# Kernel tuning notes

Hardware: AMD Instinct MI355X
Metric: run time of the kernel (lower is better)

## Reference

```python
import jax, jax.numpy as jnp
import numpy as np

B, NQ, NK, DQ, DK, D = 32, 1024, 2048, 256, 256, 256


def setup_inputs() -> dict:
    key = jax.random.key(0)
    ks = jax.random.split(key, 12)
    s = lambda fan_in: 1.0 / np.sqrt(fan_in)
    return {
        "query_input": jax.random.normal(ks[0], (B, NQ, DQ), jnp.float32),
        "key_input": jax.random.normal(ks[1], (B, NK, DK), jnp.float32),
        "value_input": jax.random.normal(ks[2], (B, NK, DK), jnp.float32),
        "query_input_mask": jax.random.randint(ks[3], (B, NQ), 0, 2).astype(jnp.int32),
        "key_input_mask": jax.random.randint(ks[4], (B, NK), 0, 2).astype(jnp.int32),
        "attn_bias": jax.random.normal(ks[5], (B, NQ, NK), jnp.float32),
        "Wq": jax.random.uniform(ks[6], (D, DQ), jnp.float32, -s(DQ), s(DQ)),
        "bq": jax.random.uniform(ks[7], (D,), jnp.float32, -s(DQ), s(DQ)),
        "Wk": jax.random.uniform(ks[8], (D, DK), jnp.float32, -s(DK), s(DK)),
        "bk": jax.random.uniform(ks[9], (D,), jnp.float32, -s(DK), s(DK)),
        "Wv": jax.random.uniform(ks[10], (D, DK), jnp.float32, -s(DK), s(DK)),
        "bv": jax.random.uniform(ks[11], (D,), jnp.float32, -s(DK), s(DK)),
    }


def reference(query_input, key_input, value_input, query_input_mask, key_input_mask,
              attn_bias, Wq, bq, Wk, bk, Wv, bv):
    scale = float(D) ** 0.5
    q = jnp.einsum("bqi,di->bqd", query_input, Wq) + bq  # (B, Nq, D)
    k = jnp.einsum("bki,di->bkd", key_input, Wk) + bk    # (B, Nk, D)
    v = jnp.einsum("bki,di->bkd", value_input, Wv) + bv  # (B, Nk, D)
    logits = jnp.einsum("bqd,bkd->bqk", q, k) / scale + attn_bias  # (B, Nq, Nk)
    # attn_mask[b,q,k] = query_mask[b,q] * key_mask[b,k]; masked_fill where == 0
    mask = (query_input_mask[:, :, None] * key_input_mask[:, None, :]) != 0
    logits = jnp.where(mask, logits, jnp.asarray(-1e9, logits.dtype))
    weights = jax.nn.softmax(logits, axis=-1)
    out = jnp.einsum("bqk,bkd->bqd", weights, v)
    return (out, weights)
```

## Files before the change

kernel.cpp:

```cpp
#include <hip/hip_runtime.h>
#include <stdint.h>

#define NB 32
#define NQd 1024
#define NKd 2048
#define DDd 256

typedef __attribute__((ext_vector_type(4))) float f32x4;
typedef __attribute__((ext_vector_type(8))) short s16x8;

__device__ __forceinline__ unsigned short f2bf(float f) {
  unsigned int u = __builtin_bit_cast(unsigned int, f);
  u += 0x7fffu + ((u >> 16) & 1u);
  return (unsigned short)(u >> 16);
}

template <int MODE>
__global__ __launch_bounds__(512) void proj_kernel(
    const float* __restrict__ P, const float* __restrict__ Q,
    const float* __restrict__ bias, unsigned short* __restrict__ out) {
  __shared__ __align__(16) char lds[32768];
  char* Pl = lds;
  char* Ql = lds + 16384;

  const int tid = threadIdx.x;
  const int m0 = blockIdx.x * 128, n0 = blockIdx.y * 128;
  const int lane = tid & 63, w = tid >> 6;
  const int lr = lane & 15, lg = lane >> 4;
  const int wm = w >> 2, wn = w & 3;

  f32x4 acc[4][2];
#pragma unroll
  for (int a = 0; a < 4; a++)
#pragma unroll
    for (int b2 = 0; b2 < 2; b2++) acc[a][b2] = (f32x4){0.f, 0.f, 0.f, 0.f};

  for (int k0 = 0; k0 < 256; k0 += 64) {
    __syncthreads();
#pragma unroll
    for (int j = 0; j < 2; j++) {
      int c = tid + j * 512;
      int row = c >> 3, cc = c & 7;
      int dst = row * 128 + ((cc * 16) ^ ((row & 7) << 4));
      {
        const float* src = P + (size_t)(m0 + row) * 256 + k0 + cc * 8;
        f32x4 x = *(const f32x4*)src;
        f32x4 y = *(const f32x4*)(src + 4);
        s16x8 pk;
        pk[0] = (short)f2bf(x[0]); pk[1] = (short)f2bf(x[1]);
        pk[2] = (short)f2bf(x[2]); pk[3] = (short)f2bf(x[3]);
        pk[4] = (short)f2bf(y[0]); pk[5] = (short)f2bf(y[1]);
        pk[6] = (short)f2bf(y[2]); pk[7] = (short)f2bf(y[3]);
        *(s16x8*)(Pl + dst) = pk;
      }
      {
        const float* src = Q + (size_t)(n0 + row) * 256 + k0 + cc * 8;
        f32x4 x = *(const f32x4*)src;
        f32x4 y = *(const f32x4*)(src + 4);
        s16x8 pk;
        pk[0] = (short)f2bf(x[0]); pk[1] = (short)f2bf(x[1]);
        pk[2] = (short)f2bf(x[2]); pk[3] = (short)f2bf(x[3]);
        pk[4] = (short)f2bf(y[0]); pk[5] = (short)f2bf(y[1]);
        pk[6] = (short)f2bf(y[2]); pk[7] = (short)f2bf(y[3]);
        *(s16x8*)(Ql + dst) = pk;
      }
    }
    __syncthreads();
#pragma unroll
    for (int ks = 0; ks < 2; ks++) {
      s16x8 af[4], bf[2];
      int kbyte = ks * 64 + lg * 16;
#pragma unroll
      for (int fm = 0; fm < 4; fm++) {
        int row = wm * 64 + fm * 16 + lr;
        af[fm] = *(const s16x8*)(Pl + row * 128 + (kbyte ^ ((row & 7) << 4)));
      }
#pragma unroll
      for (int fn = 0; fn < 2; fn++) {
        int row = wn * 32 + fn * 16 + lr;
        bf[fn] = *(const s16x8*)(Ql + row * 128 + (kbyte ^ ((row & 7) << 4)));
      }
#pragma unroll
      for (int fm = 0; fm < 4; fm++)
#pragma unroll
        for (int fn = 0; fn < 2; fn++)
          acc[fm][fn] = __builtin_amdgcn_mfma_f32_16x16x32_bf16(
              af[fm], bf[fn], acc[fm][fn], 0, 0, 0);
    }
  }

  if (MODE == 0) {
    float bv[2];
#pragma unroll
    for (int fn = 0; fn < 2; fn++) bv[fn] = bias[n0 + wn * 32 + fn * 16 + lr];
#pragma unroll
    for (int fm = 0; fm < 4; fm++)
#pragma unroll
      for (int i = 0; i < 4; i++) {
        int m = m0 + wm * 64 + fm * 16 + lg * 4 + i;
#pragma unroll
        for (int fn = 0; fn < 2; fn++) {
          int n = n0 + wn * 32 + fn * 16 + lr;
          out[(size_t)m * 256 + n] = f2bf(acc[fm][fn][i] + bv[fn]);
        }
      }
  } else {
#pragma unroll
    for (int fm = 0; fm < 4; fm++)
#pragma unroll
      for (int i = 0; i < 4; i++) {
        int m = m0 + wm * 64 + fm * 16 + lg * 4 + i;
        float bm = bias[m];
#pragma unroll
        for (int fn = 0; fn < 2; fn++) {
          int n = n0 + wn * 32 + fn * 16 + lr;
          int bb = n >> 11, nn = n & 2047;
          out[(size_t)bb * 524288 + (size_t)m * 2048 + nn] =
              f2bf(acc[fm][fn][i] + bm);
        }
      }
  }
}

__global__ __launch_bounds__(512) void attn_kernel(
    const unsigned short* __restrict__ qb, const unsigned short* __restrict__ kb,
    const unsigned short* __restrict__ vT, const int* __restrict__ qmask,
    const int* __restrict__ kmask, const float* __restrict__ bias,
    float* __restrict__ out, float* __restrict__ weights,
    float* __restrict__ rowsum_ws) {
  __shared__ __align__(16) char lds[65536];
  char* Kl = lds;
  char* Vl = lds + 32768;
  char* Sl = lds;
  float* rowsum_lds = (float*)lds;

  int bid = blockIdx.x;
  int swz = (bid & 7) * 64 + (bid >> 3);
  int b = swz >> 4, qt = swz & 15;
  int q0 = qt * 64;
  const int tid = threadIdx.x, lane = tid & 63, w = tid >> 6;
  const int lr = lane & 15, lg = lane >> 4;
  const int wm = w >> 2, wn = w & 3;

  s16x8 qf[2][8];
  {
    const unsigned short* qbase =
        qb + (size_t)(b * 1024 + q0 + wm * 32 + lr) * 256 + lg * 8;
#pragma unroll
    for (int fm = 0; fm < 2; fm++)
#pragma unroll
      for (int ks = 0; ks < 8; ks++)
        qf[fm][ks] = *(const s16x8*)(qbase + fm * 16 * 256 + ks * 32);
  }
  unsigned qmbits = 0;
#pragma unroll
  for (int fm = 0; fm < 2; fm++)
#pragma unroll
    for (int i = 0; i < 4; i++) {
      int qm = qmask[b * 1024 + q0 + wm * 32 + fm * 16 + lg * 4 + i];
      qmbits |= (qm ? 1u : 0u) << (fm * 4 + i);
    }

  f32x4 acc_o[2][4];
#pragma unroll
  for (int a = 0; a < 2; a++)
#pragma unroll
    for (int c = 0; c < 4; c++) acc_o[a][c] = (f32x4){0.f, 0.f, 0.f, 0.f};
  float rs[2][4];
#pragma unroll
  for (int a = 0; a < 2; a++)
#pragma unroll
    for (int i = 0; i < 4; i++) rs[a][i] = 0.f;

  const size_t kb_base = (size_t)b * 2048 * 256;
  const size_t vT_base = (size_t)b * 256 * 2048;

  for (int kt = 0; kt < 32; kt++) {
    __syncthreads();
#pragma unroll
    for (int j = 0; j < 4; j++) {
      int c = tid + j * 512;
      {
        int row = c >> 5, cb = (c & 31) * 16;
        s16x8 kv = *(const s16x8*)(kb + kb_base +
                                   (size_t)(kt * 64 + row) * 256 + (cb >> 1));
        *(s16x8*)(Kl + row * 512 + (cb ^ ((row & 7) << 4))) = kv;
      }
      {
        int row = c >> 3, cb = (c & 7) * 16;
        s16x8 vv = *(const s16x8*)(vT + vT_base + (size_t)row * 2048 +
                                   kt * 64 + (cb >> 1));
        *(s16x8*)(Vl + row * 128 + (cb ^ ((row & 7) << 4))) = vv;
      }
    }
    __syncthreads();
    f32x4 sacc[2];
    sacc[0] = (f32x4){0.f, 0.f, 0.f, 0.f};
    sacc[1] = (f32x4){0.f, 0.f, 0.f, 0.f};
    {
      int krow = wn * 16 + lr;
      int swzk = (krow & 7) << 4;
#pragma unroll
      for (int ks = 0; ks < 8; ks++) {
        s16x8 bfr = *(const s16x8*)(Kl + krow * 512 + ((ks * 64 + lg * 16) ^ swzk));
        sacc[0] = __builtin_amdgcn_mfma_f32_16x16x32_bf16(qf[0][ks], bfr, sacc[0], 0, 0, 0);
        sacc[1] = __builtin_amdgcn_mfma_f32_16x16x32_bf16(qf[1][ks], bfr, sacc[1], 0, 0, 0);
      }
    }
    __syncthreads();
    {
      int kcol = kt * 64 + wn * 16 + lr;
      int km = kmask[b * 2048 + kcol];
#pragma unroll
      for (int fm = 0; fm < 2; fm++)
#pragma unroll
        for (int i = 0; i < 4; i++) {
          int qrow = q0 + wm * 32 + fm * 16 + lg * 4 + i;
          float lgt = sacc[fm][i] * 0.0625f +
                      bias[((size_t)b * 1024 + qrow) * 2048 + kcol];
          float s;
          if (!((qmbits >> (fm * 4 + i)) & 1u))
            s = 1.0f;
          else
            s = km ? __expf(lgt) : 0.0f;
          rs[fm][i] += s;
          weights[((size_t)b * 1024 + qrow) * 2048 + kcol] = s;
          int srow = wm * 32 + fm * 16 + lg * 4 + i;
          int scol2 = (wn * 16 + lr) * 2;
          int sbyte = srow * 128 + ((scol2 & ~15) ^ ((srow & 7) << 4)) + (scol2 & 15);
          *(unsigned short*)(Sl + sbyte) = f2bf(s);
        }
    }
    __syncthreads();
#pragma unroll
    for (int ks = 0; ks < 2; ks++) {
      int kbyte = ks * 64 + lg * 16;
      s16x8 af[2], bfr[4];
#pragma unroll
      for (int fm = 0; fm < 2; fm++) {
        int row = wm * 32 + fm * 16 + lr;
        af[fm] = *(const s16x8*)(Sl + row * 128 + (kbyte ^ ((row & 7) << 4)));
      }
#pragma unroll
      for (int fn = 0; fn < 4; fn++) {
        int row = wn * 64 + fn * 16 + lr;
        bfr[fn] = *(const s16x8*)(Vl + row * 128 + (kbyte ^ ((row & 7) << 4)));
      }
#pragma unroll
      for (int fm = 0; fm < 2; fm++)
#pragma unroll
        for (int fn = 0; fn < 4; fn++)
          acc_o[fm][fn] = __builtin_amdgcn_mfma_f32_16x16x32_bf16(
              af[fm], bfr[fn], acc_o[fm][fn], 0, 0, 0);
    }
  }
  __syncthreads();
  if (tid < 64) rowsum_lds[tid] = 0.f;
  __syncthreads();
#pragma unroll
  for (int fm = 0; fm < 2; fm++)
#pragma unroll
    for (int i = 0; i < 4; i++) {
      float v = rs[fm][i];
      v += __shfl_xor(v, 1);
      v += __shfl_xor(v, 2);
      v += __shfl_xor(v, 4);
      v += __shfl_xor(v, 8);
      if (lr == 0) atomicAdd(&rowsum_lds[wm * 32 + fm * 16 + lg * 4 + i], v);
    }
  __syncthreads();
#pragma unroll
  for (int fm = 0; fm < 2; fm++)
#pragma unroll
    for (int i = 0; i < 4; i++) {
      int srow = wm * 32 + fm * 16 + lg * 4 + i;
      float rinv = 1.0f / rowsum_lds[srow];
      int qrow = q0 + srow;
#pragma unroll
      for (int fn = 0; fn < 4; fn++) {
        int d = wn * 64 + fn * 16 + lr;
        out[((size_t)b * 1024 + qrow) * 256 + d] = acc_o[fm][fn][i] * rinv;
      }
    }
  if (tid < 64) rowsum_ws[b * 1024 + q0 + tid] = rowsum_lds[tid];
}

__global__ __launch_bounds__(256) void rescale_kernel(
    float* __restrict__ weights, const float* __restrict__ rowsum) {
  const size_t total = (size_t)32 * 1024 * 2048 / 4;
  size_t stride = (size_t)gridDim.x * blockDim.x;
  for (size_t i = (size_t)blockIdx.x * blockDim.x + threadIdx.x; i < total;
       i += stride) {
    size_t row = i >> 9;
    float rinv = 1.0f / rowsum[row];
    f32x4 v = ((const f32x4*)weights)[i];
    v[0] *= rinv; v[1] *= rinv; v[2] *= rinv; v[3] *= rinv;
    ((f32x4*)weights)[i] = v;
  }
}

extern "C" void kernel_launch(void* const* d_in, const int* in_sizes, int n_in,
                              void* d_out, int out_size, void* d_ws,
                              size_t ws_size, hipStream_t stream) {
  const float* query = (const float*)d_in[0];
  const float* key = (const float*)d_in[1];
  const float* value = (const float*)d_in[2];
  const int* qmask = (const int*)d_in[3];
  const int* kmask = (const int*)d_in[4];
  const float* bias = (const float*)d_in[5];
  const float* Wq = (const float*)d_in[6];
  const float* bq = (const float*)d_in[7];
  const float* Wk = (const float*)d_in[8];
  const float* bk = (const float*)d_in[9];
  const float* Wv = (const float*)d_in[10];
  const float* bv = (const float*)d_in[11];

  float* out = (float*)d_out;
  float* weights = out + (size_t)32 * 1024 * 256;

  char* ws = (char*)d_ws;
  unsigned short* qb = (unsigned short*)ws;
  unsigned short* kbb = (unsigned short*)(ws + 16777216);
  unsigned short* vT = (unsigned short*)(ws + 50331648);
  float* rowsum = (float*)(ws + 83886080);

  proj_kernel<0><<<dim3(256, 2), 512, 0, stream>>>(query, Wq, bq, qb);
  proj_kernel<0><<<dim3(512, 2), 512, 0, stream>>>(key, Wk, bk, kbb);
  proj_kernel<1><<<dim3(2, 512), 512, 0, stream>>>(Wv, value, bv, vT);
  attn_kernel<<<dim3(512), 512, 0, stream>>>(qb, kbb, vT, qmask, kmask, bias,
                                             out, weights, rowsum);
  rescale_kernel<<<dim3(2048), 256, 0, stream>>>(weights, rowsum);
}
```

Baseline: 872.4 us.

## Stage logits through LDS for coalesced vectorized bias loads and weight stores

The attention kernel now writes raw QK scores to a rotated fp32 LDS tile and re-reads them in a row-major layout, so each thread handles four contiguous columns of one row. Bias loads, mask loads and weight stores become 16-byte coalesced nontemporal accesses, and the bias for the next tile is prefetched. The row sum is reduced with a short shuffle, and the kernel stores reciprocals so the rescale pass avoids divisions. This costs an extra LDS round-trip and barrier per tile, and adds a minBlocks launch bound that may constrain registers.

```diff
diff --git a/kernel.cpp b/kernel.cpp
--- a/kernel.cpp
+++ b/kernel.cpp
@@ -1,13 +1,10 @@
 #include <hip/hip_runtime.h>
 #include <stdint.h>
 
-#define NB 32
-#define NQd 1024
-#define NKd 2048
-#define DDd 256
-
 typedef __attribute__((ext_vector_type(4))) float f32x4;
 typedef __attribute__((ext_vector_type(8))) short s16x8;
+typedef __attribute__((ext_vector_type(4))) short s16x4;
+typedef __attribute__((ext_vector_type(4))) int i32x4;
 
 __device__ __forceinline__ unsigned short f2bf(float f) {
   unsigned int u = __builtin_bit_cast(unsigned int, f);
@@ -122,16 +119,17 @@
   }
 }
 
-__global__ __launch_bounds__(512) void attn_kernel(
+__global__ __launch_bounds__(512, 4) void attn_kernel(
     const unsigned short* __restrict__ qb, const unsigned short* __restrict__ kb,
     const unsigned short* __restrict__ vT, const int* __restrict__ qmask,
     const int* __restrict__ kmask, const float* __restrict__ bias,
     float* __restrict__ out, float* __restrict__ weights,
-    float* __restrict__ rowsum_ws) {
+    float* __restrict__ rowrecip_ws) {
   __shared__ __align__(16) char lds[65536];
   char* Kl = lds;
   char* Vl = lds + 32768;
-  char* Sl = lds;
+  char* Sf = lds;
+  char* Sl = lds + 16384;
   float* rowsum_lds = (float*)lds;
 
   int bid = blockIdx.x;
@@ -142,6 +140,14 @@
   const int lr = lane & 15, lg = lane >> 4;
   const int wm = w >> 2, wn = w & 3;
 
+  const int pr = tid >> 3, pc = tid & 7;
+  const int qrow_pb = b * 1024 + q0 + pr;
+  const int qm_pb = qmask[qrow_pb];
+  const float* bias_row = bias + (size_t)qrow_pb * 2048;
+  float* wrow = weights + (size_t)qrow_pb * 2048;
+  const int* kmask_b = kmask + b * 2048;
+  const int prot = ((pr >> 2) & 3) * 64;
+
   s16x8 qf[2][8];
   {
     const unsigned short* qbase =
@@ -152,28 +158,19 @@
       for (int ks = 0; ks < 8; ks++)
         qf[fm][ks] = *(const s16x8*)(qbase + fm * 16 * 256 + ks * 32);
   }
-  unsigned qmbits = 0;
-#pragma unroll
-  for (int fm = 0; fm < 2; fm++)
-#pragma unroll
-    for (int i = 0; i < 4; i++) {
-      int qm = qmask[b * 1024 + q0 + wm * 32 + fm * 16 + lg * 4 + i];
-      qmbits |= (qm ? 1u : 0u) << (fm * 4 + i);
-    }
 
   f32x4 acc_o[2][4];
 #pragma unroll
   for (int a = 0; a < 2; a++)
 #pragma unroll
     for (int c = 0; c < 4; c++) acc_o[a][c] = (f32x4){0.f, 0.f, 0.f, 0.f};
-  float rs[2][4];
-#pragma unroll
-  for (int a = 0; a < 2; a++)
-#pragma unroll
-    for (int i = 0; i < 4; i++) rs[a][i] = 0.f;
+  float rs = 0.f;
 
   const size_t kb_base = (size_t)b * 2048 * 256;
   const size_t vT_base = (size_t)b * 256 * 2048;
+
+  f32x4 bcur0 = __builtin_nontemporal_load((const f32x4*)(bias_row + pc * 4));
+  f32x4 bcur1 = __builtin_nontemporal_load((const f32x4*)(bias_row + (pc + 8) * 4));
 
   for (int kt = 0; kt < 32; kt++) {
     __syncthreads();
@@ -209,27 +206,49 @@
     }
     __syncthreads();
     {
-      int kcol = kt * 64 + wn * 16 + lr;
-      int km = kmask[b * 2048 + kcol];
+      int col4 = (wn * 16 + lr) * 4;
 #pragma unroll
       for (int fm = 0; fm < 2; fm++)
 #pragma unroll
         for (int i = 0; i < 4; i++) {
-          int qrow = q0 + wm * 32 + fm * 16 + lg * 4 + i;
-          float lgt = sacc[fm][i] * 0.0625f +
-                      bias[((size_t)b * 1024 + qrow) * 2048 + kcol];
-          float s;
-          if (!((qmbits >> (fm * 4 + i)) & 1u))
-            s = 1.0f;
-          else
-            s = km ? __expf(lgt) : 0.0f;
-          rs[fm][i] += s;
-          weights[((size_t)b * 1024 + qrow) * 2048 + kcol] = s;
-          int srow = wm * 32 + fm * 16 + lg * 4 + i;
-          int scol2 = (wn * 16 + lr) * 2;
-          int sbyte = srow * 128 + ((scol2 & ~15) ^ ((srow & 7) << 4)) + (scol2 & 15);
-          *(unsigned short*)(Sl + sbyte) = f2bf(s);
+          int row = wm * 32 + fm * 16 + lg * 4 + i;
+          *(float*)(Sf + row * 256 + ((col4 + ((row >> 2) & 3) * 64) & 255)) =
+              sacc[fm][i];
         }
+    }
+    __syncthreads();
+    {
+      int ktn = (kt + 1) & 31;
+      f32x4 bn0 = __builtin_nontemporal_load(
+          (const f32x4*)(bias_row + ktn * 64 + pc * 4));
+      f32x4 bn1 = __builtin_nontemporal_load(
+          (const f32x4*)(bias_row + ktn * 64 + (pc + 8) * 4));
+#pragma unroll
+      for (int half = 0; half < 2; half++) {
+        int c = pc + half * 8;
+        f32x4 bv = half ? bcur1 : bcur0;
+        f32x4 sv = *(const f32x4*)(Sf + pr * 256 + ((c * 16 + prot) & 255));
+        i32x4 kmv = *(const i32x4*)(kmask_b + kt * 64 + c * 4);
+        f32x4 sval;
+#pragma unroll
+        for (int j = 0; j < 4; j++) {
+          float lgt = sv[j] * 0.0625f + bv[j];
+          float e = kmv[j] ? __expf(lgt) : 0.0f;
+          sval[j] = qm_pb ? e : 1.0f;
+        }
+        rs += sval[0] + sval[1] + sval[2] + sval[3];
+        __builtin_nontemporal_store(sval, (f32x4*)(wrow + kt * 64 + c * 4));
+        s16x4 h;
+        h[0] = (short)f2bf(sval[0]);
+        h[1] = (short)f2bf(sval[1]);
+        h[2] = (short)f2bf(sval[2]);
+        h[3] = (short)f2bf(sval[3]);
+        int cb = c * 8;
+        int sb = pr * 128 + ((cb & ~15) ^ ((pr & 7) << 4)) + (cb & 15);
+        *(s16x4*)(Sl + sb) = h;
+      }
+      bcur0 = bn0;
+      bcur1 = bn1;
     }
     __syncthreads();
 #pragma unroll
@@ -254,27 +273,24 @@
               af[fm], bfr[fn], acc_o[fm][fn], 0, 0, 0);
     }
   }
-  __syncthreads();
-  if (tid < 64) rowsum_lds[tid] = 0.f;
-  __syncthreads();
-#pragma unroll
-  for (int fm = 0; fm < 2; fm++)
-#pragma unroll
-    for (int i = 0; i < 4; i++) {
-      float v = rs[fm][i];
-      v += __shfl_xor(v, 1);
-      v += __shfl_xor(v, 2);
-      v += __shfl_xor(v, 4);
-      v += __shfl_xor(v, 8);
-      if (lr == 0) atomicAdd(&rowsum_lds[wm * 32 + fm * 16 + lg * 4 + i], v);
-    }
+  {
+    float tot = rs;
+    tot += __shfl_xor(tot, 1);
+    tot += __shfl_xor(tot, 2);
+    tot += __shfl_xor(tot, 4);
+    float rinv = 1.0f / tot;
+    if ((tid & 7) == 0) {
+      rowsum_lds[pr] = rinv;
+      rowrecip_ws[b * 1024 + q0 + pr] = rinv;
+    }
+  }
   __syncthreads();
 #pragma unroll
   for (int fm = 0; fm < 2; fm++)
 #pragma unroll
     for (int i = 0; i < 4; i++) {
       int srow = wm * 32 + fm * 16 + lg * 4 + i;
-      float rinv = 1.0f / rowsum_lds[srow];
+      float rinv = rowsum_lds[srow];
       int qrow = q0 + srow;
 #pragma unroll
       for (int fn = 0; fn < 4; fn++) {
@@ -282,20 +298,19 @@
         out[((size_t)b * 1024 + qrow) * 256 + d] = acc_o[fm][fn][i] * rinv;
       }
     }
-  if (tid < 64) rowsum_ws[b * 1024 + q0 + tid] = rowsum_lds[tid];
 }
 
 __global__ __launch_bounds__(256) void rescale_kernel(
-    float* __restrict__ weights, const float* __restrict__ rowsum) {
+    float* __restrict__ weights, const float* __restrict__ rinvarr) {
   const size_t total = (size_t)32 * 1024 * 2048 / 4;
   size_t stride = (size_t)gridDim.x * blockDim.x;
   for (size_t i = (size_t)blockIdx.x * blockDim.x + threadIdx.x; i < total;
        i += stride) {
     size_t row = i >> 9;
-    float rinv = 1.0f / rowsum[row];
-    f32x4 v = ((const f32x4*)weights)[i];
+    float rinv = rinvarr[row];
+    f32x4 v = __builtin_nontemporal_load((const f32x4*)weights + i);
     v[0] *= rinv; v[1] *= rinv; v[2] *= rinv; v[3] *= rinv;
-    ((f32x4*)weights)[i] = v;
+    __builtin_nontemporal_store(v, (f32x4*)weights + i);
   }
 }
 
@@ -322,12 +337,12 @@
   unsigned short* qb = (unsigned short*)ws;
   unsigned short* kbb = (unsigned short*)(ws + 16777216);
   unsigned short* vT = (unsigned short*)(ws + 50331648);
-  float* rowsum = (float*)(ws + 83886080);
+  float* rowrecip = (float*)(ws + 83886080);
 
   proj_kernel<0><<<dim3(256, 2), 512, 0, stream>>>(query, Wq, bq, qb);
   proj_kernel<0><<<dim3(512, 2), 512, 0, stream>>>(key, Wk, bk, kbb);
   proj_kernel<1><<<dim3(2, 512), 512, 0, stream>>>(Wv, value, bv, vT);
   attn_kernel<<<dim3(512), 512, 0, stream>>>(qb, kbb, vT, qmask, kmask, bias,
-                                             out, weights, rowsum);
-  rescale_kernel<<<dim3(2048), 256, 0, stream>>>(weights, rowsum);
-}
+                                             out, weights, rowrecip);
+  rescale_kernel<<<dim3(2048), 256, 0, stream>>>(weights, rowrecip);
+}
```

Result: slower. 1.077 ms (+23.4%).
